# Kernel tuning notes

Measured on AMD Instinct MI355X. Metric: run time of the kernel, lower is better.

## Reference

```python
import jax, jax.numpy as jnp
import numpy as np

TEMPERATURE = 10.0
EPS = 1e-12  # torch F.normalize eps


def setup_inputs() -> dict:
    key = jax.random.key(0)
    k1, k2 = jax.random.split(key)
    B, D = 8192, 1024
    text_embeddings = jax.random.normal(k1, (B, D), dtype=jnp.float32)
    image_embeddings = jax.random.normal(k2, (B, D), dtype=jnp.float32)
    bias = jnp.zeros((1,), dtype=jnp.float32)
    return {
        "text_embeddings": text_embeddings,
        "image_embeddings": image_embeddings,
        "bias": bias,
    }


def _normalize(x):
    # matches torch F.normalize(p=2, dim=1): x / max(||x||, eps)
    norm = jnp.linalg.norm(x, axis=-1, keepdims=True)
    return x / jnp.maximum(norm, EPS)


def reference(text_embeddings, image_embeddings, bias):
    B = text_embeddings.shape[0]
    img_n = _normalize(image_embeddings)   # [B, D]
    txt_n = _normalize(text_embeddings)    # [B, D]
    # similarity[i, j] = <img_i, txt_j>
    sim = jnp.einsum('id,jd->ij', img_n, txt_n)          # [B, B]
    logits = sim * (-TEMPERATURE) + bias[0]
    labels = 2.0 * jnp.eye(B, dtype=logits.dtype) - 1.0   # +1 diag, -1 off-diag
    # loss_ij = log(1/(1+exp(label*logit))) = -softplus(label*logit)
    total_loss = -jnp.sum(jax.nn.softplus(labels * logits))
    return -(total_loss / B)
```

## Files before the change

### kernel.cpp

```cpp
#include <hip/hip_runtime.h>
#include <stdint.h>
#include <stddef.h>

#define NROWS 8192
#define DIM   1024
#define RB    512
#define TEMP  10.0f

#define BM 256
#define BN 256
#define BK 128

typedef __attribute__((ext_vector_type(8))) int i32x8;
typedef __attribute__((ext_vector_type(16))) float floatx16;

__device__ __forceinline__ void load16_lds(const unsigned char* g, unsigned char* l) {
    __builtin_amdgcn_global_load_lds(
        (__attribute__((address_space(1))) void*)(g),
        (__attribute__((address_space(3))) void*)(l),
        16, 0, 0);
}

__device__ __forceinline__ unsigned fp4q(float x) {
    float a = fabsf(x);
    a = fminf(a, 6.0f);
    unsigned c = (unsigned)(a >= 0.25f) + (unsigned)(a >= 0.75f)
               + (unsigned)(a >= 1.25f) + (unsigned)(a >= 1.75f)
               + (unsigned)(a >= 2.5f)  + (unsigned)(a >= 3.5f)
               + (unsigned)(a >= 5.0f);
    return c | ((__float_as_uint(x) >> 28) & 8u);
}

__device__ __forceinline__ i32x8 op8(int4 lo) {
    union { i32x8 v; int4 q[2]; } u;
    u.q[0] = lo;
    u.q[1] = make_int4(0, 0, 0, 0);
    return u.v;
}

__global__ __launch_bounds__(256) void normalize_kernel(
    const float* __restrict__ img, const float* __restrict__ txt,
    unsigned char* __restrict__ imgq, unsigned char* __restrict__ txtq,
    float* __restrict__ out)
{
    const int gw = blockIdx.x * 4 + (threadIdx.x >> 6);
    const int lane = threadIdx.x & 63;
    const float* src;
    unsigned char* dst;
    if (gw < NROWS) {
        src = img + (size_t)gw * DIM;
        dst = imgq + (size_t)gw * RB;
    } else {
        src = txt + (size_t)(gw - NROWS) * DIM;
        dst = txtq + (size_t)(gw - NROWS) * RB;
    }
    float4 v[4];
    float ss = 0.f;
#pragma unroll
    for (int c = 0; c < 4; c++) {
        v[c] = ((const float4*)src)[lane + 64 * c];
        ss += v[c].x * v[c].x + v[c].y * v[c].y + v[c].z * v[c].z + v[c].w * v[c].w;
    }
#pragma unroll
    for (int off = 32; off; off >>= 1) ss += __shfl_xor(ss, off);
    const float scale = 32.0f / fmaxf(sqrtf(ss), 1e-12f);
#pragma unroll
    for (int c = 0; c < 4; c++) {
        unsigned p = fp4q(v[c].x * scale)
                   | (fp4q(v[c].y * scale) << 4)
                   | (fp4q(v[c].z * scale) << 8)
                   | (fp4q(v[c].w * scale) << 12);
        ((unsigned short*)dst)[lane + 64 * c] = (unsigned short)p;
    }
    if (gw == 0 && lane == 0) out[0] = 0.f;
}

__global__ __launch_bounds__(512, 1) void simloss_kernel(
    const unsigned char* __restrict__ An,
    const unsigned char* __restrict__ Bn,
    const float* __restrict__ bias,
    float* __restrict__ out)
{
    __shared__ unsigned char As[2][BM * 64];
    __shared__ unsigned char Bs[2][BN * 64];
    __shared__ float red[24];

    const int t = threadIdx.x;
    const int lane = t & 63;
    const int wave = t >> 6;

    const int bid = blockIdx.x;
    const int blockN = (bid & 7) + 8 * ((bid >> 3) & 3);
    const int blockM = bid >> 5;

    int rowS[2], chS[2];
#pragma unroll
    for (int i = 0; i < 2; i++) {
        const int S = t + i * 512;
        const int pair = S >> 3, s7 = S & 7;
        rowS[i] = 2 * pair + (s7 & 1);
        chS[i] = ((s7 >> 1) ^ pair) & 3;
    }
    const unsigned char* gA0 = An + (size_t)(blockM * BM + rowS[0]) * RB + chS[0] * 16;
    const unsigned char* gA1 = An + (size_t)(blockM * BM + rowS[1]) * RB + chS[1] * 16;
    const unsigned char* gB0 = Bn + (size_t)(blockN * BN + rowS[0]) * RB + chS[0] * 16;
    const unsigned char* gB1 = Bn + (size_t)(blockN * BN + rowS[1]) * RB + chS[1] * 16;

    const int waveM = (wave >> 2) * 128;
    const int waveN = (wave & 3) * 64;
    const int fr = lane & 31;
    const int fh = lane >> 5;
    const int qk = (fr >> 1) & 3;
    const int po = 128 * (fr >> 1) + 16 * (fr & 1);
    const int offc0 = 32 * ((fh ^ qk) & 3);

    floatx16 acc[4][2];
#pragma unroll
    for (int mi = 0; mi < 4; mi++)
#pragma unroll
        for (int ni = 0; ni < 2; ni++)
            acc[mi][ni] = (floatx16)(0.f);

    load16_lds(gA0, &As[0][t * 16]);
    load16_lds(gA1, &As[0][t * 16 + 8192]);
    load16_lds(gB0, &Bs[0][t * 16]);
    load16_lds(gB1, &Bs[0][t * 16 + 8192]);

#pragma unroll
    for (int it = 0; it < DIM / BK; it++) {
        const int cur = it & 1;
        __syncthreads();
        if (it < DIM / BK - 1) {
            const int kb = (it + 1) * 64;
            load16_lds(gA0 + kb, &As[cur ^ 1][t * 16]);
            load16_lds(gA1 + kb, &As[cur ^ 1][t * 16 + 8192]);
            load16_lds(gB0 + kb, &Bs[cur ^ 1][t * 16]);
            load16_lds(gB1 + kb, &Bs[cur ^ 1][t * 16 + 8192]);
        }

        asm volatile("s_setprio 1");
#pragma unroll
        for (int ks = 0; ks < 2; ks++) {
            const int offc = offc0 ^ (ks << 6);
            int4 b[2];
#pragma unroll
            for (int ni = 0; ni < 2; ni++)
                b[ni] = *(const int4*)&Bs[cur][64 * (waveN + 32 * ni) + po + offc];
#pragma unroll
            for (int mi = 0; mi < 4; mi++) {
                int4 a = *(const int4*)&As[cur][64 * (waveM + 32 * mi) + po + offc];
#pragma unroll
                for (int ni = 0; ni < 2; ni++)
                    acc[mi][ni] = __builtin_amdgcn_mfma_scale_f32_32x32x64_f8f6f4(
                        op8(a), op8(b[ni]), acc[mi][ni],
                        4, 4,
                        0, 0x7f7f7f7f,
                        0, 0x7f7f7f7f);
            }
        }
        asm volatile("s_setprio 0");
    }

    const float bv = bias[0];
    const float c1 = -TEMP * 1.4426950408889634f / 1024.0f;
    const float c0 = bv * 1.4426950408889634f;
    float accP = 0.f, accQ = 0.f, accD = 0.f;
    const int gi0 = blockM * BM + waveM + 4 * fh;
    const int gj0 = blockN * BN + waveN + fr;
#pragma unroll
    for (int mi = 0; mi < 4; mi++) {
#pragma unroll
        for (int ni = 0; ni < 2; ni++) {
#pragma unroll
            for (int reg = 0; reg < 16; reg++) {
                float s = acc[mi][ni][reg];
                float w = fmaf(s, c1, c0);
                float e2 = __builtin_amdgcn_exp2f(-fabsf(w));
                accP += __builtin_amdgcn_logf(1.0f + e2);
                accP = fmaf(0.5f, fabsf(w), accP);
                accQ += s;
            }
        }
    }
    const bool diagblk = (blockN == blockM);
    if (diagblk) {
#pragma unroll
        for (int mi = 0; mi < 4; mi++)
#pragma unroll
            for (int ni = 0; ni < 2; ni++)
#pragma unroll
                for (int reg = 0; reg < 16; reg++) {
                    int ig = gi0 + mi * 32 + (reg & 3) + 8 * (reg >> 2);
                    int jg = gj0 + ni * 32;
                    if (ig == jg) accD += acc[mi][ni][reg];
                }
    }
#pragma unroll
    for (int off = 32; off; off >>= 1) {
        accP += __shfl_xor(accP, off);
        accQ += __shfl_xor(accQ, off);
        accD += __shfl_xor(accD, off);
    }
    if (lane == 0) {
        red[wave * 3 + 0] = accP;
        red[wave * 3 + 1] = accQ;
        red[wave * 3 + 2] = accD;
    }
    __syncthreads();
    if (t == 0) {
        float P = 0.f, Q = 0.f, D = 0.f;
#pragma unroll
        for (int w = 0; w < 8; w++) {
            P += red[w * 3 + 0];
            Q += red[w * 3 + 1];
            D += red[w * 3 + 2];
        }
        Q *= (1.0f / 1024.0f);
        D *= (1.0f / 1024.0f);
        float contrib = fmaf(0.6931471805599453f, P, fmaf(5.0f, Q, -32768.0f * bv));
        if (diagblk) contrib += fmaf(-TEMP, D, 256.0f * bv);
        atomicAdd(out, contrib * (1.0f / 8192.0f));
    }
}

extern "C" void kernel_launch(void* const* d_in, const int* in_sizes, int n_in,
                              void* d_out, int out_size, void* d_ws, size_t ws_size,
                              hipStream_t stream) {
    const float* txt = (const float*)d_in[0];
    const float* img = (const float*)d_in[1];
    const float* bias = (const float*)d_in[2];
    float* out = (float*)d_out;

    unsigned char* imgq = (unsigned char*)d_ws;
    unsigned char* txtq = imgq + (size_t)NROWS * RB;

    normalize_kernel<<<dim3(2 * NROWS / 4), dim3(256), 0, stream>>>(
        img, txt, imgq, txtq, out);

    simloss_kernel<<<dim3((NROWS / BM) * (NROWS / BN)), dim3(512), 0, stream>>>(
        imgq, txtq, bias, out);
}
```

Before: 150.9 us.

## Pre-swizzle FP4 operands into MFMA fragment layout and drop LDS staging

The normalize kernel now writes the FP4-quantized rows directly in the per-lane MFMA operand layout, as 32-row by 64-element chunks of 1 KB. The GEMM kernel then loads its fragments straight from global memory into registers and skips the LDS double-buffer and barriers. The tile shrinks to 256x128 per block with 4 waves and 2 blocks per CU, which doubles the grid. This removes LDS traffic and syncs, but operand reuse now depends on L2 and cache hits, and global load latency is not explicitly pipelined.

```diff
diff --git a/kernel.cpp b/kernel.cpp
--- a/kernel.cpp
+++ b/kernel.cpp
@@ -4,22 +4,12 @@
 
 #define NROWS 8192
 #define DIM   1024
-#define RB    512
+#define NQ    16
 #define TEMP  10.0f
 
-#define BM 256
-#define BN 256
-#define BK 128
 
 typedef __attribute__((ext_vector_type(8))) int i32x8;
 typedef __attribute__((ext_vector_type(16))) float floatx16;
-
-__device__ __forceinline__ void load16_lds(const unsigned char* g, unsigned char* l) {
-    __builtin_amdgcn_global_load_lds(
-        (__attribute__((address_space(1))) void*)(g),
-        (__attribute__((address_space(3))) void*)(l),
-        16, 0, 0);
-}
 
 __device__ __forceinline__ unsigned fp4q(float x) {
     float a = fabsf(x);
@@ -31,13 +21,6 @@
     return c | ((__float_as_uint(x) >> 28) & 8u);
 }
 
-__device__ __forceinline__ i32x8 op8(int4 lo) {
-    union { i32x8 v; int4 q[2]; } u;
-    u.q[0] = lo;
-    u.q[1] = make_int4(0, 0, 0, 0);
-    return u.v;
-}
-
 __global__ __launch_bounds__(256) void normalize_kernel(
     const float* __restrict__ img, const float* __restrict__ txt,
     unsigned char* __restrict__ imgq, unsigned char* __restrict__ txtq,
@@ -47,72 +30,61 @@
     const int lane = threadIdx.x & 63;
     const float* src;
     unsigned char* dst;
+    int row;
     if (gw < NROWS) {
-        src = img + (size_t)gw * DIM;
-        dst = imgq + (size_t)gw * RB;
+        row = gw;
+        src = img + (size_t)row * DIM;
+        dst = imgq;
     } else {
-        src = txt + (size_t)(gw - NROWS) * DIM;
-        dst = txtq + (size_t)(gw - NROWS) * RB;
+        row = gw - NROWS;
+        src = txt + (size_t)row * DIM;
+        dst = txtq;
     }
     float4 v[4];
     float ss = 0.f;
 #pragma unroll
     for (int c = 0; c < 4; c++) {
-        v[c] = ((const float4*)src)[lane + 64 * c];
+        v[c] = ((const float4*)src)[lane * 4 + c];
         ss += v[c].x * v[c].x + v[c].y * v[c].y + v[c].z * v[c].z + v[c].w * v[c].w;
     }
 #pragma unroll
     for (int off = 32; off; off >>= 1) ss += __shfl_xor(ss, off);
     const float scale = 32.0f / fmaxf(sqrtf(ss), 1e-12f);
+    unsigned p[4];
 #pragma unroll
-    for (int c = 0; c < 4; c++) {
-        unsigned p = fp4q(v[c].x * scale)
-                   | (fp4q(v[c].y * scale) << 4)
-                   | (fp4q(v[c].z * scale) << 8)
-                   | (fp4q(v[c].w * scale) << 12);
-        ((unsigned short*)dst)[lane + 64 * c] = (unsigned short)p;
-    }
+    for (int c = 0; c < 4; c++)
+        p[c] = fp4q(v[c].x * scale)
+             | (fp4q(v[c].y * scale) << 4)
+             | (fp4q(v[c].z * scale) << 8)
+             | (fp4q(v[c].w * scale) << 12);
+    uint2 o = make_uint2(p[0] | (p[1] << 16), p[2] | (p[3] << 16));
+    const int r = row >> 5, w = row & 31;
+    const int q = lane >> 2, h = (lane >> 1) & 1, par = lane & 1;
+    const size_t destb = (size_t)(r * 16 + q) * 1024 + (w + 32 * h) * 16 + 8 * par;
+    *(uint2*)(dst + destb) = o;
     if (gw == 0 && lane == 0) out[0] = 0.f;
 }
 
-__global__ __launch_bounds__(512, 1) void simloss_kernel(
+__global__ __launch_bounds__(256, 2) void simloss_kernel(
     const unsigned char* __restrict__ An,
     const unsigned char* __restrict__ Bn,
     const float* __restrict__ bias,
     float* __restrict__ out)
 {
-    __shared__ unsigned char As[2][BM * 64];
-    __shared__ unsigned char Bs[2][BN * 64];
-    __shared__ float red[24];
-
     const int t = threadIdx.x;
     const int lane = t & 63;
     const int wave = t >> 6;
 
     const int bid = blockIdx.x;
-    const int blockN = (bid & 7) + 8 * ((bid >> 3) & 3);
-    const int blockM = bid >> 5;
+    const int blockN = (bid & 7) + 8 * ((bid >> 3) & 7);
+    const int blockM = bid >> 6;
 
-    int rowS[2], chS[2];
-#pragma unroll
-    for (int i = 0; i < 2; i++) {
-        const int S = t + i * 512;
-        const int pair = S >> 3, s7 = S & 7;
-        rowS[i] = 2 * pair + (s7 & 1);
-        chS[i] = ((s7 >> 1) ^ pair) & 3;
-    }
-    const unsigned char* gA0 = An + (size_t)(blockM * BM + rowS[0]) * RB + chS[0] * 16;
-    const unsigned char* gA1 = An + (size_t)(blockM * BM + rowS[1]) * RB + chS[1] * 16;
-    const unsigned char* gB0 = Bn + (size_t)(blockN * BN + rowS[0]) * RB + chS[0] * 16;
-    const unsigned char* gB1 = Bn + (size_t)(blockN * BN + rowS[1]) * RB + chS[1] * 16;
-
-    const int waveM = (wave >> 2) * 128;
-    const int waveN = (wave & 3) * 64;
-    const int fr = lane & 31;
-    const int fh = lane >> 5;
-    const int qk = (fr >> 1) & 3;
-    const int po = 128 * (fr >> 1) + 16 * (fr & 1);
-    const int offc0 = 32 * ((fh ^ qk) & 3);
+    const int waveM2 = wave >> 1;
+    const int waveN2 = wave & 1;
+    const int rA0 = blockM * 8 + waveM2 * 4;
+    const int rB0 = blockN * 4 + waveN2 * 2;
+    const unsigned char* pA = An + (size_t)rA0 * 16 * 1024 + lane * 16;
+    const unsigned char* pB = Bn + (size_t)rB0 * 16 * 1024 + lane * 16;
 
     floatx16 acc[4][2];
 #pragma unroll
@@ -121,52 +93,40 @@
         for (int ni = 0; ni < 2; ni++)
             acc[mi][ni] = (floatx16)(0.f);
 
-    load16_lds(gA0, &As[0][t * 16]);
-    load16_lds(gA1, &As[0][t * 16 + 8192]);
-    load16_lds(gB0, &Bs[0][t * 16]);
-    load16_lds(gB1, &Bs[0][t * 16 + 8192]);
+    union U { i32x8 v; int4 q[2]; };
+    U ua[4], ub[2];
+#pragma unroll
+    for (int mi = 0; mi < 4; mi++) ua[mi].v = (i32x8)(0);
+#pragma unroll
+    for (int ni = 0; ni < 2; ni++) ub[ni].v = (i32x8)(0);
 
 #pragma unroll
-    for (int it = 0; it < DIM / BK; it++) {
-        const int cur = it & 1;
-        __syncthreads();
-        if (it < DIM / BK - 1) {
-            const int kb = (it + 1) * 64;
-            load16_lds(gA0 + kb, &As[cur ^ 1][t * 16]);
-            load16_lds(gA1 + kb, &As[cur ^ 1][t * 16 + 8192]);
-            load16_lds(gB0 + kb, &Bs[cur ^ 1][t * 16]);
-            load16_lds(gB1 + kb, &Bs[cur ^ 1][t * 16 + 8192]);
-        }
-
-        asm volatile("s_setprio 1");
+    for (int q = 0; q < NQ; q++) {
 #pragma unroll
-        for (int ks = 0; ks < 2; ks++) {
-            const int offc = offc0 ^ (ks << 6);
-            int4 b[2];
+        for (int ni = 0; ni < 2; ni++)
+            ub[ni].q[0] = *(const int4*)(pB + (((size_t)ni * 16 + q) << 10));
+#pragma unroll
+        for (int mi = 0; mi < 4; mi++)
+            ua[mi].q[0] = *(const int4*)(pA + (((size_t)mi * 16 + q) << 10));
+#pragma unroll
+        for (int mi = 0; mi < 4; mi++)
 #pragma unroll
             for (int ni = 0; ni < 2; ni++)
-                b[ni] = *(const int4*)&Bs[cur][64 * (waveN + 32 * ni) + po + offc];
-#pragma unroll
-            for (int mi = 0; mi < 4; mi++) {
-                int4 a = *(const int4*)&As[cur][64 * (waveM + 32 * mi) + po + offc];
-#pragma unroll
-                for (int ni = 0; ni < 2; ni++)
-                    acc[mi][ni] = __builtin_amdgcn_mfma_scale_f32_32x32x64_f8f6f4(
-                        op8(a), op8(b[ni]), acc[mi][ni],
-                        4, 4,
-                        0, 0x7f7f7f7f,
-                        0, 0x7f7f7f7f);
-            }
-        }
-        asm volatile("s_setprio 0");
+                acc[mi][ni] = __builtin_amdgcn_mfma_scale_f32_32x32x64_f8f6f4(
+                    ua[mi].v, ub[ni].v, acc[mi][ni],
+                    4, 4,
+                    0, 0x7f7f7f7f,
+                    0, 0x7f7f7f7f);
     }
 
     const float bv = bias[0];
     const float c1 = -TEMP * 1.4426950408889634f / 1024.0f;
     const float c0 = bv * 1.4426950408889634f;
     float accP = 0.f, accQ = 0.f, accD = 0.f;
-    const int gi0 = blockM * BM + waveM + 4 * fh;
-    const int gj0 = blockN * BN + waveN + fr;
+    const int fr = lane & 31;
+    const int fh = lane >> 5;
+    const int gi0 = blockM * 256 + waveM2 * 128 + 4 * fh;
+    const int gj0 = blockN * 128 + waveN2 * 64 + fr;
 #pragma unroll
     for (int mi = 0; mi < 4; mi++) {
 #pragma unroll
@@ -182,7 +142,7 @@
             }
         }
     }
-    const bool diagblk = (blockN == blockM);
+    const bool diagblk = ((blockN >> 1) == blockM);
     if (diagblk) {
 #pragma unroll
         for (int mi = 0; mi < 4; mi++)
@@ -201,6 +161,7 @@
         accQ += __shfl_xor(accQ, off);
         accD += __shfl_xor(accD, off);
     }
+    __shared__ float red[12];
     if (lane == 0) {
         red[wave * 3 + 0] = accP;
         red[wave * 3 + 1] = accQ;
@@ -208,17 +169,13 @@
     }
     __syncthreads();
     if (t == 0) {
-        float P = 0.f, Q = 0.f, D = 0.f;
-#pragma unroll
-        for (int w = 0; w < 8; w++) {
-            P += red[w * 3 + 0];
-            Q += red[w * 3 + 1];
-            D += red[w * 3 + 2];
-        }
+        float P = red[0] + red[3] + red[6] + red[9];
+        float Q = red[1] + red[4] + red[7] + red[10];
+        float D = red[2] + red[5] + red[8] + red[11];
         Q *= (1.0f / 1024.0f);
         D *= (1.0f / 1024.0f);
-        float contrib = fmaf(0.6931471805599453f, P, fmaf(5.0f, Q, -32768.0f * bv));
-        if (diagblk) contrib += fmaf(-TEMP, D, 256.0f * bv);
+        float contrib = fmaf(0.6931471805599453f, P, fmaf(5.0f, Q, -16384.0f * bv));
+        if (diagblk) contrib += fmaf(-TEMP, D, 128.0f * bv);
         atomicAdd(out, contrib * (1.0f / 8192.0f));
     }
 }
@@ -232,11 +189,11 @@
     float* out = (float*)d_out;
 
     unsigned char* imgq = (unsigned char*)d_ws;
-    unsigned char* txtq = imgq + (size_t)NROWS * RB;
+    unsigned char* txtq = imgq + (size_t)NROWS * (DIM / 2);
 
     normalize_kernel<<<dim3(2 * NROWS / 4), dim3(256), 0, stream>>>(
         img, txt, imgq, txtq, out);
 
-    simloss_kernel<<<dim3((NROWS / BM) * (NROWS / BN)), dim3(512), 0, stream>>>(
+    simloss_kernel<<<dim3(32 * 64), dim3(256), 0, stream>>>(
         imgq, txtq, bias, out);
 }
```

After: 158.3 us. 4.9% more time.
